# Performance work log

Measured on AMD Instinct MI355X. Metric: run time of the kernel, lower is better.

The kernel has to match this reference:

```python
import jax, jax.numpy as jnp
import numpy as np
import math

B, N, D = 2, 4096, 1024
NUM_LAYERS = 12
INIT_RANGE = 0.02


def setup_inputs() -> dict:
    key = jax.random.key(0)
    k1, k2 = jax.random.split(key)
    hidden_states = jax.random.normal(k1, (B, N, D), dtype=jnp.float32)
    std = INIT_RANGE / math.sqrt(2.0 * NUM_LAYERS * D)
    queries = jax.random.normal(k2, (D, D), dtype=jnp.float32) * std
    return {"hidden_states": hidden_states, "queries": queries}


def reference(hidden_states, queries):
    # Q = F.linear(X, W) = X @ W^T  -> [B, N, D]
    q = jnp.einsum('bnd,ed->bne', hidden_states, queries)
    # pre_attn = Q @ X^T  -> [B, N, N]
    pre_attn = jnp.einsum('bne,bme->bnm', q, hidden_states)
    # attention = pre_attn @ X  -> [B, N, D]
    attention = jnp.einsum('bnm,bmd->bnd', pre_attn, hidden_states)
    return attention
```

## Files before the change

kernel.cpp:

```cpp
#include <hip/hip_runtime.h>
#include <hip/hip_bf16.h>
#include <stdint.h>

using bf16 = __hip_bfloat16;
typedef __attribute__((ext_vector_type(8))) short short8;
typedef __attribute__((ext_vector_type(4))) float f32x4;

#define BM 128
#define BK 32

__device__ __forceinline__ void g2lds16(const void* g, void* l) {
    __builtin_amdgcn_global_load_lds(
        (const __attribute__((address_space(1))) void*)g,
        (__attribute__((address_space(3))) void*)l,
        16, 0, 0);
}

__device__ __forceinline__ short f2bs(float x) {
    union { bf16 h; short s; } u;
    u.h = __float2bfloat16(x);
    return u.s;
}

__device__ __forceinline__ int bswz(int row, int cg) { return cg ^ ((row >> 1) & 3); }
__device__ __forceinline__ int fswz(int row, int cg) { return cg ^ (row & 7); }

__global__ __launch_bounds__(256)
void transpose_cvt(const float* __restrict__ src, ushort* __restrict__ dstT,
                   ushort* __restrict__ dstN,
                   int R, int C, long sstride, long dstrideT, long dstrideN)
{
    __shared__ __align__(16) ushort t[64][72];
    const float* s = src + (size_t)blockIdx.z * sstride;
    ushort*      dT = dstT + (size_t)blockIdx.z * dstrideT;
    const int r0 = blockIdx.y * 64, c0 = blockIdx.x * 64;
    const int tid = threadIdx.x;
#pragma unroll
    for (int ii = 0; ii < 4; ++ii) {
        int idx = ii * 256 + tid;
        int r = idx >> 4, c4 = (idx & 15) * 4;
        float4 v = *(const float4*)&s[(size_t)(r0 + r) * C + c0 + c4];
        union { ushort u[4]; uint2 q; } o;
        o.u[0] = (ushort)f2bs(v.x); o.u[1] = (ushort)f2bs(v.y);
        o.u[2] = (ushort)f2bs(v.z); o.u[3] = (ushort)f2bs(v.w);
        *(uint2*)&t[r][c4] = o.q;
        if (dstN) {
            ushort* dN = dstN + (size_t)blockIdx.z * dstrideN;
            *(uint2*)&dN[(size_t)(r0 + r) * C + c0 + c4] = o.q;
        }
    }
    __syncthreads();
#pragma unroll
    for (int ii = 0; ii < 2; ++ii) {
        int idx = ii * 256 + tid;
        int c = idx >> 3, r8 = (idx & 7) * 8;
        union { ushort u[8]; uint4 v; } tmp;
#pragma unroll
        for (int j = 0; j < 8; ++j) tmp.u[j] = t[r8 + j][c];
        *(uint4*)&dT[(size_t)(c0 + c) * R + r0 + r8] = tmp.v;
    }
}

__global__ __launch_bounds__(256)
void cvt_f32_bf16(const float* __restrict__ in, ushort* __restrict__ out, int n4)
{
    int i = blockIdx.x * 256 + threadIdx.x;
    if (i >= n4) return;
    float4 v = ((const float4*)in)[i];
    union { ushort u[4]; uint2 q; } o;
    o.u[0] = (ushort)f2bs(v.x); o.u[1] = (ushort)f2bs(v.y);
    o.u[2] = (ushort)f2bs(v.z); o.u[3] = (ushort)f2bs(v.w);
    ((uint2*)out)[i] = o.q;
}

template <int MODE, int A_F32, int NFRAG>
__global__ __launch_bounds__(256)
void gemm_bt(const void* __restrict__ Av, const bf16* __restrict__ B,
             void* __restrict__ Cv, int M, int N, int K, int kChunks,
             long sA, long sB, long sC)
{
    constexpr int BN  = 32 * NFRAG;
    constexpr int BSH = BN / 64;
    __shared__ __align__(16) bf16 lA[BM * BK * (A_F32 ? 2 : 1)];
    __shared__ __align__(16) bf16 lB[BN * BK];

    const int z     = blockIdx.z;
    const int batch = z / kChunks;
    const int chunk = z - batch * kChunks;
    const int kLen  = K / kChunks;
    const int k0    = chunk * kLen;

    const int m0 = blockIdx.y * BM;
    const int n0 = blockIdx.x * BN;

    const int tid  = threadIdx.x;
    const int lane = tid & 63;
    const int wave = tid >> 6;
    const int wr   = wave >> 1, wc = wave & 1;
    const int ml   = lane & 15;
    const int q    = lane >> 4;

    const bf16* Bb = B + (size_t)batch * sB;
    const bf16* bp[BSH];
#pragma unroll
    for (int s = 0; s < BSH; ++s) {
        int idx = s * 256 + tid;
        int row = idx >> 2, cg = idx & 3;
        bp[s] = Bb + (size_t)(n0 + row) * K + k0 + 8 * bswz(row, cg);
    }

    const float* a32[4];
    const bf16*  a16[2];
    if constexpr (A_F32) {
        const float* Ab = (const float*)Av + (size_t)batch * sA;
#pragma unroll
        for (int s = 0; s < 4; ++s) {
            int idx = s * 256 + tid;
            int row = idx >> 3, cg = idx & 7;
            a32[s] = Ab + (size_t)(m0 + row) * K + k0 + 4 * fswz(row, cg);
        }
    } else {
        const bf16* Ab = (const bf16*)Av + (size_t)batch * sA;
#pragma unroll
        for (int s = 0; s < 2; ++s) {
            int idx = s * 256 + tid;
            int row = idx >> 2, cg = idx & 3;
            a16[s] = Ab + (size_t)(m0 + row) * K + k0 + 8 * bswz(row, cg);
        }
    }

    f32x4 acc[4][NFRAG] = {};

    const int nk = kLen / BK;
    for (int kt = 0; kt < nk; ++kt) {
        if constexpr (A_F32) {
            float* lAf = (float*)lA;
#pragma unroll
            for (int s = 0; s < 4; ++s) {
                g2lds16(a32[s], &lAf[(s * 256 + tid) * 4]);
                a32[s] += BK;
            }
        } else {
#pragma unroll
            for (int s = 0; s < 2; ++s) {
                g2lds16(a16[s], &lA[(s * 256 + tid) * 8]);
                a16[s] += BK;
            }
        }
#pragma unroll
        for (int s = 0; s < BSH; ++s) {
            g2lds16(bp[s], &lB[(s * 256 + tid) * 8]);
            bp[s] += BK;
        }
        __syncthreads();

        short8 af[4], bfr[NFRAG];
#pragma unroll
        for (int i = 0; i < 4; ++i) {
            const int rA = wr * 64 + i * 16 + ml;
            if constexpr (A_F32) {
                const float* lAf = (const float*)lA;
                float4 x0 = *(const float4*)&lAf[rA * 32 + 4 * fswz(rA, 2 * q)];
                float4 x1 = *(const float4*)&lAf[rA * 32 + 4 * fswz(rA, 2 * q + 1)];
                af[i][0] = f2bs(x0.x); af[i][1] = f2bs(x0.y);
                af[i][2] = f2bs(x0.z); af[i][3] = f2bs(x0.w);
                af[i][4] = f2bs(x1.x); af[i][5] = f2bs(x1.y);
                af[i][6] = f2bs(x1.z); af[i][7] = f2bs(x1.w);
            } else {
                af[i] = *(const short8*)&lA[rA * 32 + 8 * bswz(rA, q)];
            }
        }
#pragma unroll
        for (int j = 0; j < NFRAG; ++j) {
            const int rB = wc * (16 * NFRAG) + j * 16 + ml;
            bfr[j] = *(const short8*)&lB[rB * 32 + 8 * bswz(rB, q)];
        }
#pragma unroll
        for (int mi = 0; mi < 4; ++mi)
#pragma unroll
            for (int nj = 0; nj < NFRAG; ++nj)
                acc[mi][nj] = __builtin_amdgcn_mfma_f32_16x16x32_bf16(
                    af[mi], bfr[nj], acc[mi][nj], 0, 0, 0);
        __syncthreads();
    }

#pragma unroll
    for (int mi = 0; mi < 4; ++mi)
#pragma unroll
        for (int nj = 0; nj < NFRAG; ++nj)
#pragma unroll
            for (int r = 0; r < 4; ++r) {
                int row = m0 + wr * 64 + mi * 16 + q * 4 + r;
                int col = n0 + wc * (16 * NFRAG) + nj * 16 + ml;
                if constexpr (MODE == 1) {
                    float* Cf = (float*)Cv + (size_t)batch * sC;
                    atomicAdd(&Cf[(size_t)row * N + col], acc[mi][nj][r]);
                } else if constexpr (MODE == 0) {
                    ushort* Cb = (ushort*)Cv + (size_t)batch * sC;
                    Cb[(size_t)row * N + col] = (ushort)f2bs(acc[mi][nj][r]);
                } else {
                    float* Cf = (float*)Cv + (size_t)batch * sC;
                    Cf[(size_t)row * N + col] = acc[mi][nj][r];
                }
            }
}

extern "C" void kernel_launch(void* const* d_in, const int* in_sizes, int n_in,
                              void* d_out, int out_size, void* d_ws, size_t ws_size,
                              hipStream_t stream)
{
    const int B = 2, N = 4096, D = 1024;
    const float* X = (const float*)d_in[0];
    const float* W = (const float*)d_in[1];
    float* out = (float*)d_out;

    char* ob = (char*)d_out;
    char* ws = (char*)d_ws;
    ushort* Xt = (ushort*)ob;
    float*  Gf = (float*)(ob + (16ll << 20));
    ushort* G  = (ushort*)(ob + (24ll << 20));
    ushort* Wt = (ushort*)(ob + (28ll << 20));

    const bool bigws = ws_size >= (20ull << 20);
    ushort* Xb = bigws ? (ushort*)ws : nullptr;
    ushort* Mt = (ushort*)(ws + (bigws ? (16ll << 20) : 0));

    transpose_cvt<<<dim3(D / 64, N / 64, B), 256, 0, stream>>>(
        X, Xt, Xb, N, D, (long)N * D, (long)D * N, (long)N * D);
    transpose_cvt<<<dim3(D / 64, D / 64, 1), 256, 0, stream>>>(
        W, Wt, nullptr, D, D, 0, 0, 0);
    (void)hipMemsetAsync(Gf, 0, (size_t)B * D * D * sizeof(float), stream);
    gemm_bt<1, 0, 2><<<dim3(D / 64, D / BM, B * 4), 256, 0, stream>>>(
        (const void*)Xt, (const bf16*)Xt, Gf, D, D, N, 4,
        (long)D * N, (long)D * N, (long)D * D);
    cvt_f32_bf16<<<dim3((B * D * D / 4 + 255) / 256), 256, 0, stream>>>(
        Gf, G, B * D * D / 4);
    gemm_bt<0, 0, 2><<<dim3(D / 64, D / BM, B), 256, 0, stream>>>(
        (const void*)G, (const bf16*)Wt, Mt, D, D, D, 1,
        (long)D * D, 0, (long)D * D);
    if (bigws) {
        gemm_bt<2, 0, 2><<<dim3(D / 64, N / BM, B), 256, 0, stream>>>(
            (const void*)Xb, (const bf16*)Mt, out, N, D, D, 1,
            (long)N * D, (long)D * D, (long)N * D);
    } else {
        gemm_bt<2, 1, 2><<<dim3(D / 64, N / BM, B), 256, 0, stream>>>(
            (const void*)X, (const bf16*)Mt, out, N, D, D, 1,
            (long)N * D, (long)D * D, (long)N * D);
    }
}
```

Baseline: 196.6 us.

## Double-buffer LDS tiles in GEMM and fuse Gram f32-to-bf16 conversion into next GEMM

Double-buffers the GEMM's shared-memory A and B tiles. The next K tile is issued with async global-to-LDS loads while the current tile is being computed, and one barrier per iteration is removed. Separately, the standalone f32-to-bf16 conversion kernel for the Gram matrix is dropped, and the second GEMM reads the f32 accumulator directly through its A_F32 path, saving a launch and a round trip through memory. In exchange, LDS use doubles, which may lower occupancy, and the f32 A path moves twice the A bytes per tile.

```diff
diff --git a/kernel.cpp b/kernel.cpp
--- a/kernel.cpp
+++ b/kernel.cpp
@@ -61,18 +61,6 @@
     }
 }
 
-__global__ __launch_bounds__(256)
-void cvt_f32_bf16(const float* __restrict__ in, ushort* __restrict__ out, int n4)
-{
-    int i = blockIdx.x * 256 + threadIdx.x;
-    if (i >= n4) return;
-    float4 v = ((const float4*)in)[i];
-    union { ushort u[4]; uint2 q; } o;
-    o.u[0] = (ushort)f2bs(v.x); o.u[1] = (ushort)f2bs(v.y);
-    o.u[2] = (ushort)f2bs(v.z); o.u[3] = (ushort)f2bs(v.w);
-    ((uint2*)out)[i] = o.q;
-}
-
 template <int MODE, int A_F32, int NFRAG>
 __global__ __launch_bounds__(256)
 void gemm_bt(const void* __restrict__ Av, const bf16* __restrict__ B,
@@ -81,8 +69,8 @@
 {
     constexpr int BN  = 32 * NFRAG;
     constexpr int BSH = BN / 64;
-    __shared__ __align__(16) bf16 lA[BM * BK * (A_F32 ? 2 : 1)];
-    __shared__ __align__(16) bf16 lB[BN * BK];
+    __shared__ __align__(16) bf16 lA[2][BM * BK * (A_F32 ? 2 : 1)];
+    __shared__ __align__(16) bf16 lB[2][BN * BK];
 
     const int z     = blockIdx.z;
     const int batch = z / kChunks;
@@ -129,12 +117,9 @@
         }
     }
 
-    f32x4 acc[4][NFRAG] = {};
-
-    const int nk = kLen / BK;
-    for (int kt = 0; kt < nk; ++kt) {
+    auto stage = [&](int buf) {
         if constexpr (A_F32) {
-            float* lAf = (float*)lA;
+            float* lAf = (float*)lA[buf];
 #pragma unroll
             for (int s = 0; s < 4; ++s) {
                 g2lds16(a32[s], &lAf[(s * 256 + tid) * 4]);
@@ -143,23 +128,32 @@
         } else {
 #pragma unroll
             for (int s = 0; s < 2; ++s) {
-                g2lds16(a16[s], &lA[(s * 256 + tid) * 8]);
+                g2lds16(a16[s], &lA[buf][(s * 256 + tid) * 8]);
                 a16[s] += BK;
             }
         }
 #pragma unroll
         for (int s = 0; s < BSH; ++s) {
-            g2lds16(bp[s], &lB[(s * 256 + tid) * 8]);
+            g2lds16(bp[s], &lB[buf][(s * 256 + tid) * 8]);
             bp[s] += BK;
         }
+    };
+
+    f32x4 acc[4][NFRAG] = {};
+
+    const int nk = kLen / BK;
+    stage(0);
+    for (int kt = 0; kt < nk; ++kt) {
+        const int cur = kt & 1;
         __syncthreads();
+        if (kt + 1 < nk) stage(cur ^ 1);
 
         short8 af[4], bfr[NFRAG];
 #pragma unroll
         for (int i = 0; i < 4; ++i) {
             const int rA = wr * 64 + i * 16 + ml;
             if constexpr (A_F32) {
-                const float* lAf = (const float*)lA;
+                const float* lAf = (const float*)lA[cur];
                 float4 x0 = *(const float4*)&lAf[rA * 32 + 4 * fswz(rA, 2 * q)];
                 float4 x1 = *(const float4*)&lAf[rA * 32 + 4 * fswz(rA, 2 * q + 1)];
                 af[i][0] = f2bs(x0.x); af[i][1] = f2bs(x0.y);
@@ -167,13 +161,13 @@
                 af[i][4] = f2bs(x1.x); af[i][5] = f2bs(x1.y);
                 af[i][6] = f2bs(x1.z); af[i][7] = f2bs(x1.w);
             } else {
-                af[i] = *(const short8*)&lA[rA * 32 + 8 * bswz(rA, q)];
+                af[i] = *(const short8*)&lA[cur][rA * 32 + 8 * bswz(rA, q)];
             }
         }
 #pragma unroll
         for (int j = 0; j < NFRAG; ++j) {
             const int rB = wc * (16 * NFRAG) + j * 16 + ml;
-            bfr[j] = *(const short8*)&lB[rB * 32 + 8 * bswz(rB, q)];
+            bfr[j] = *(const short8*)&lB[cur][rB * 32 + 8 * bswz(rB, q)];
         }
 #pragma unroll
         for (int mi = 0; mi < 4; ++mi)
@@ -181,7 +175,6 @@
             for (int nj = 0; nj < NFRAG; ++nj)
                 acc[mi][nj] = __builtin_amdgcn_mfma_f32_16x16x32_bf16(
                     af[mi], bfr[nj], acc[mi][nj], 0, 0, 0);
-        __syncthreads();
     }
 
 #pragma unroll
@@ -218,7 +211,6 @@
     char* ws = (char*)d_ws;
     ushort* Xt = (ushort*)ob;
     float*  Gf = (float*)(ob + (16ll << 20));
-    ushort* G  = (ushort*)(ob + (24ll << 20));
     ushort* Wt = (ushort*)(ob + (28ll << 20));
 
     const bool bigws = ws_size >= (20ull << 20);
@@ -233,10 +225,8 @@
     gemm_bt<1, 0, 2><<<dim3(D / 64, D / BM, B * 4), 256, 0, stream>>>(
         (const void*)Xt, (const bf16*)Xt, Gf, D, D, N, 4,
         (long)D * N, (long)D * N, (long)D * D);
-    cvt_f32_bf16<<<dim3((B * D * D / 4 + 255) / 256), 256, 0, stream>>>(
-        Gf, G, B * D * D / 4);
-    gemm_bt<0, 0, 2><<<dim3(D / 64, D / BM, B), 256, 0, stream>>>(
-        (const void*)G, (const bf16*)Wt, Mt, D, D, D, 1,
+    gemm_bt<0, 1, 2><<<dim3(D / 64, D / BM, B), 256, 0, stream>>>(
+        (const void*)Gf, (const bf16*)Wt, Mt, D, D, D, 1,
         (long)D * D, 0, (long)D * D);
     if (bigws) {
         gemm_bt<2, 0, 2><<<dim3(D / 64, N / BM, B), 256, 0, stream>>>(
```

New measurement: 198.6 us. Within noise of the previous version (+1.0%).

## Pre-pack bf16 operands into MFMA fragment layout and add LDS-free wave GEMM

Applied to the files above, without the earlier changes.

The transpose kernel now writes X^T and X in a packed layout where each 16-row by 32-k MFMA fragment is stored contiguously per lane. A new single-wave GEMM reads those fragments straight from global memory without LDS or barriers, and is used for the Gram split-K product and the final product. The separate fp32-to-bf16 conversion pass is dropped: the middle GEMM reads the fp32 Gram matrix directly, converts it in registers, and writes its result in packed form. This removes one kernel launch and the LDS staging and sync overhead. The cost is no cross-wave reuse through LDS, so each small block does more global or L2 traffic.

```diff
diff --git a/kernel.cpp b/kernel.cpp
--- a/kernel.cpp
+++ b/kernel.cpp
@@ -25,10 +25,12 @@
 __device__ __forceinline__ int bswz(int row, int cg) { return cg ^ ((row >> 1) & 3); }
 __device__ __forceinline__ int fswz(int row, int cg) { return cg ^ (row & 7); }
 
+
 __global__ __launch_bounds__(256)
 void transpose_cvt(const float* __restrict__ src, ushort* __restrict__ dstT,
                    ushort* __restrict__ dstN,
-                   int R, int C, long sstride, long dstrideT, long dstrideN)
+                   int R, int C, long sstride, long dstrideT, long dstrideN,
+                   int packT)
 {
     __shared__ __align__(16) ushort t[64][72];
     const float* s = src + (size_t)blockIdx.z * sstride;
@@ -46,7 +48,10 @@
         *(uint2*)&t[r][c4] = o.q;
         if (dstN) {
             ushort* dN = dstN + (size_t)blockIdx.z * dstrideN;
-            *(uint2*)&dN[(size_t)(r0 + r) * C + c0 + c4] = o.q;
+            int m = r0 + r, k = c0 + c4;
+            int lane = (m & 15) + 16 * ((k >> 3) & 3);
+            size_t pidx = (((size_t)(m >> 4) * (C >> 5) + (k >> 5)) * 64 + lane) * 8 + (k & 7);
+            *(uint2*)&dN[pidx] = o.q;
         }
     }
     __syncthreads();
@@ -57,20 +62,15 @@
         union { ushort u[8]; uint4 v; } tmp;
 #pragma unroll
         for (int j = 0; j < 8; ++j) tmp.u[j] = t[r8 + j][c];
-        *(uint4*)&dT[(size_t)(c0 + c) * R + r0 + r8] = tmp.v;
-    }
-}
-
-__global__ __launch_bounds__(256)
-void cvt_f32_bf16(const float* __restrict__ in, ushort* __restrict__ out, int n4)
-{
-    int i = blockIdx.x * 256 + threadIdx.x;
-    if (i >= n4) return;
-    float4 v = ((const float4*)in)[i];
-    union { ushort u[4]; uint2 q; } o;
-    o.u[0] = (ushort)f2bs(v.x); o.u[1] = (ushort)f2bs(v.y);
-    o.u[2] = (ushort)f2bs(v.z); o.u[3] = (ushort)f2bs(v.w);
-    ((uint2*)out)[i] = o.q;
+        if (packT) {
+            int m = c0 + c, k = r0 + r8;
+            int lane = (m & 15) + 16 * ((k >> 3) & 3);
+            size_t pidx = (((size_t)(m >> 4) * (R >> 5) + (k >> 5)) * 64 + lane) * 8;
+            *(uint4*)&dT[pidx] = tmp.v;
+        } else {
+            *(uint4*)&dT[(size_t)(c0 + c) * R + r0 + r8] = tmp.v;
+        }
+    }
 }
 
 template <int MODE, int A_F32, int NFRAG>
@@ -89,10 +89,8 @@
     const int chunk = z - batch * kChunks;
     const int kLen  = K / kChunks;
     const int k0    = chunk * kLen;
-
     const int m0 = blockIdx.y * BM;
     const int n0 = blockIdx.x * BN;
-
     const int tid  = threadIdx.x;
     const int lane = tid & 63;
     const int wave = tid >> 6;
@@ -130,28 +128,18 @@
     }
 
     f32x4 acc[4][NFRAG] = {};
-
     const int nk = kLen / BK;
     for (int kt = 0; kt < nk; ++kt) {
         if constexpr (A_F32) {
             float* lAf = (float*)lA;
 #pragma unroll
-            for (int s = 0; s < 4; ++s) {
-                g2lds16(a32[s], &lAf[(s * 256 + tid) * 4]);
-                a32[s] += BK;
-            }
+            for (int s = 0; s < 4; ++s) { g2lds16(a32[s], &lAf[(s * 256 + tid) * 4]); a32[s] += BK; }
         } else {
 #pragma unroll
-            for (int s = 0; s < 2; ++s) {
-                g2lds16(a16[s], &lA[(s * 256 + tid) * 8]);
-                a16[s] += BK;
-            }
-        }
-#pragma unroll
-        for (int s = 0; s < BSH; ++s) {
-            g2lds16(bp[s], &lB[(s * 256 + tid) * 8]);
-            bp[s] += BK;
-        }
+            for (int s = 0; s < 2; ++s) { g2lds16(a16[s], &lA[(s * 256 + tid) * 8]); a16[s] += BK; }
+        }
+#pragma unroll
+        for (int s = 0; s < BSH; ++s) { g2lds16(bp[s], &lB[(s * 256 + tid) * 8]); bp[s] += BK; }
         __syncthreads();
 
         short8 af[4], bfr[NFRAG];
@@ -198,6 +186,74 @@
                 } else if constexpr (MODE == 0) {
                     ushort* Cb = (ushort*)Cv + (size_t)batch * sC;
                     Cb[(size_t)row * N + col] = (ushort)f2bs(acc[mi][nj][r]);
+                } else if constexpr (MODE == 3) {
+                    ushort* Cb = (ushort*)Cv + (size_t)batch * sC;
+                    int plane = (row & 15) + 16 * ((col >> 3) & 3);
+                    size_t pidx = (((size_t)(row >> 4) * (N >> 5) + (col >> 5)) * 64 + plane) * 8 + (col & 7);
+                    Cb[pidx] = (ushort)f2bs(acc[mi][nj][r]);
+                } else {
+                    float* Cf = (float*)Cv + (size_t)batch * sC;
+                    Cf[(size_t)row * N + col] = acc[mi][nj][r];
+                }
+            }
+}
+
+template <int MODE, int MFRAG, int NFRAG>
+__global__ __launch_bounds__(64, 2)
+void gemm_wp(const ushort* __restrict__ Ap, const ushort* __restrict__ Bp,
+             void* __restrict__ Cv, int N, int K, int kChunks,
+             long sA, long sB, long sC)
+{
+    const int z      = blockIdx.z;
+    const int batch  = z / kChunks;
+    const int chunk  = z - batch * kChunks;
+    const int ktiles = K >> 5;
+    const int nkt    = ktiles / kChunks;
+    const int kt0    = chunk * nkt;
+    const int m0     = blockIdx.y * (MFRAG * 16);
+    const int n0     = blockIdx.x * (NFRAG * 16);
+    const int lane   = threadIdx.x;
+
+    const ushort* Ab = Ap + (size_t)batch * sA;
+    const ushort* Bb = Bp + (size_t)batch * sB;
+    const ushort* ap[MFRAG];
+    const ushort* bp[NFRAG];
+#pragma unroll
+    for (int f = 0; f < MFRAG; ++f)
+        ap[f] = Ab + (((size_t)((m0 >> 4) + f) * ktiles + kt0) * 64 + lane) * 8;
+#pragma unroll
+    for (int f = 0; f < NFRAG; ++f)
+        bp[f] = Bb + (((size_t)((n0 >> 4) + f) * ktiles + kt0) * 64 + lane) * 8;
+
+    f32x4 acc[MFRAG][NFRAG] = {};
+
+#pragma unroll 4
+    for (int kt = 0; kt < nkt; ++kt) {
+        short8 af[MFRAG], bfr[NFRAG];
+#pragma unroll
+        for (int f = 0; f < MFRAG; ++f) { af[f]  = *(const short8*)ap[f]; ap[f] += 512; }
+#pragma unroll
+        for (int f = 0; f < NFRAG; ++f) { bfr[f] = *(const short8*)bp[f]; bp[f] += 512; }
+#pragma unroll
+        for (int mi = 0; mi < MFRAG; ++mi)
+#pragma unroll
+            for (int nj = 0; nj < NFRAG; ++nj)
+                acc[mi][nj] = __builtin_amdgcn_mfma_f32_16x16x32_bf16(
+                    af[mi], bfr[nj], acc[mi][nj], 0, 0, 0);
+    }
+
+    const int ml = lane & 15, q = lane >> 4;
+#pragma unroll
+    for (int mi = 0; mi < MFRAG; ++mi)
+#pragma unroll
+        for (int nj = 0; nj < NFRAG; ++nj)
+#pragma unroll
+            for (int r = 0; r < 4; ++r) {
+                int row = m0 + mi * 16 + q * 4 + r;
+                int col = n0 + nj * 16 + ml;
+                if constexpr (MODE == 1) {
+                    float* Cf = (float*)Cv + (size_t)batch * sC;
+                    atomicAdd(&Cf[(size_t)row * N + col], acc[mi][nj][r]);
                 } else {
                     float* Cf = (float*)Cv + (size_t)batch * sC;
                     Cf[(size_t)row * N + col] = acc[mi][nj][r];
@@ -218,7 +274,6 @@
     char* ws = (char*)d_ws;
     ushort* Xt = (ushort*)ob;
     float*  Gf = (float*)(ob + (16ll << 20));
-    ushort* G  = (ushort*)(ob + (24ll << 20));
     ushort* Wt = (ushort*)(ob + (28ll << 20));
 
     const bool bigws = ws_size >= (20ull << 20);
@@ -226,23 +281,22 @@
     ushort* Mt = (ushort*)(ws + (bigws ? (16ll << 20) : 0));
 
     transpose_cvt<<<dim3(D / 64, N / 64, B), 256, 0, stream>>>(
-        X, Xt, Xb, N, D, (long)N * D, (long)D * N, (long)N * D);
+        X, Xt, Xb, N, D, (long)N * D, (long)D * N, (long)N * D, 1);
     transpose_cvt<<<dim3(D / 64, D / 64, 1), 256, 0, stream>>>(
-        W, Wt, nullptr, D, D, 0, 0, 0);
+        W, Wt, nullptr, D, D, 0, 0, 0, 0);
     (void)hipMemsetAsync(Gf, 0, (size_t)B * D * D * sizeof(float), stream);
-    gemm_bt<1, 0, 2><<<dim3(D / 64, D / BM, B * 4), 256, 0, stream>>>(
-        (const void*)Xt, (const bf16*)Xt, Gf, D, D, N, 4,
-        (long)D * N, (long)D * N, (long)D * D);
-    cvt_f32_bf16<<<dim3((B * D * D / 4 + 255) / 256), 256, 0, stream>>>(
-        Gf, G, B * D * D / 4);
-    gemm_bt<0, 0, 2><<<dim3(D / 64, D / BM, B), 256, 0, stream>>>(
-        (const void*)G, (const bf16*)Wt, Mt, D, D, D, 1,
-        (long)D * D, 0, (long)D * D);
+    gemm_wp<1, 4, 4><<<dim3(D / 64, D / 64, B * 4), 64, 0, stream>>>(
+        Xt, Xt, Gf, D, N, 4, (long)D * N, (long)D * N, (long)D * D);
     if (bigws) {
-        gemm_bt<2, 0, 2><<<dim3(D / 64, N / BM, B), 256, 0, stream>>>(
-            (const void*)Xb, (const bf16*)Mt, out, N, D, D, 1,
-            (long)N * D, (long)D * D, (long)N * D);
+        gemm_bt<3, 1, 2><<<dim3(D / 64, D / BM, B), 256, 0, stream>>>(
+            (const void*)Gf, (const bf16*)Wt, Mt, D, D, D, 1,
+            (long)D * D, 0, (long)D * D);
+        gemm_wp<2, 4, 4><<<dim3(D / 64, N / 64, B), 64, 0, stream>>>(
+            Xb, Mt, out, D, D, 1, (long)N * D, (long)D * D, (long)N * D);
     } else {
+        gemm_bt<0, 1, 2><<<dim3(D / 64, D / BM, B), 256, 0, stream>>>(
+            (const void*)Gf, (const bf16*)Wt, Mt, D, D, D, 1,
+            (long)D * D, 0, (long)D * D);
         gemm_bt<2, 1, 2><<<dim3(D / 64, N / BM, B), 256, 0, stream>>>(
             (const void*)X, (const bf16*)Mt, out, N, D, D, 1,
             (long)N * D, (long)D * D, (long)N * D);
```

New measurement: 235.6 us. +19.9%, slower.
